# Kernel tuning notes

Measured on AMD Instinct MI355X. Metric: run time of the kernel, lower is better.

## Reference

```python
import jax, jax.numpy as jnp
import numpy as np

B, S, D, H, R = 4, 1024, 1024, 16, 4
HD = D // H
EPS = 1e-5


def layer_norm(x, g, b):
    mu = jnp.mean(x, axis=-1, keepdims=True)
    var = jnp.mean(jnp.square(x - mu), axis=-1, keepdims=True)
    return (x - mu) * jax.lax.rsqrt(var + EPS) * g + b


def setup_inputs() -> dict:
    key = jax.random.key(0)
    ks = jax.random.split(key, 12)
    sd = 1.0 / np.sqrt(D)
    sf = 1.0 / np.sqrt(R * D)
    inp = {
        "x": jax.random.normal(ks[0], (B, S, D), jnp.float32),
        "ln1_g": jnp.ones((D,), jnp.float32),
        "ln1_b": jnp.zeros((D,), jnp.float32),
        "wq": jax.random.uniform(ks[1], (D, D), jnp.float32, -sd, sd),
        "bq": jnp.zeros((D,), jnp.float32),
        "wk": jax.random.uniform(ks[2], (D, D), jnp.float32, -sd, sd),
        "bk": jnp.zeros((D,), jnp.float32),
        "wv": jax.random.uniform(ks[3], (D, D), jnp.float32, -sd, sd),
        "bv": jnp.zeros((D,), jnp.float32),
        "wo": jax.random.uniform(ks[4], (D, D), jnp.float32, -sd, sd),
        "bo": jnp.zeros((D,), jnp.float32),
        "ln2_g": jnp.ones((D,), jnp.float32),
        "ln2_b": jnp.zeros((D,), jnp.float32),
        "w1": jax.random.uniform(ks[5], (D, R * D), jnp.float32, -sd, sd),
        "b1": jnp.zeros((R * D,), jnp.float32),
        "w2": jax.random.uniform(ks[6], (R * D, D), jnp.float32, -sf, sf),
        "b2": jnp.zeros((D,), jnp.float32),
    }
    return inp


def reference(x, ln1_g, ln1_b, wq, bq, wk, bk, wv, bv, wo, bo,
              ln2_g, ln2_b, w1, b1, w2, b2):
    # Pre-LN MHA. Per-head Q/K/V linears concatenated == one batched projection
    # reshaped into heads, so we batch all heads in single GEMMs.
    h = layer_norm(x, ln1_g, ln1_b)
    q = (h @ wq + bq).reshape(B, S, H, HD)
    k = (h @ wk + bk).reshape(B, S, H, HD)
    v = (h @ wv + bv).reshape(B, S, H, HD)
    scores = jnp.einsum("bqhd,bkhd->bhqk", q, k) / np.sqrt(HD)
    attn = jax.nn.softmax(scores, axis=-1)
    ctx = jnp.einsum("bhqk,bkhd->bqhd", attn, v).reshape(B, S, D)
    x = x + ctx @ wo + bo
    # Pre-LN MLP with exact (erf) GELU, matching torch nn.GELU default.
    h2 = layer_norm(x, ln2_g, ln2_b)
    mlp = jax.nn.gelu(h2 @ w1 + b1, approximate=False) @ w2 + b2
    return x + mlp
```

## Files before the change

### kernel.cpp

```cpp
#include <hip/hip_runtime.h>

typedef unsigned short u16;
typedef __attribute__((ext_vector_type(8))) __bf16 bf16x8;
typedef __attribute__((ext_vector_type(4))) float floatx4;

#define FLAG_F32OUT  1
#define FLAG_GELU    2
#define FLAG_PARTIAL 4
#define FLAG_PBF16   8

__device__ __forceinline__ u16 f2bf(float f) {
  union { float f; unsigned u; } un;
  un.f = f;
  unsigned u = un.u;
  u += 0x7fffu + ((u >> 16) & 1u);
  return (u16)(u >> 16);
}

__device__ __forceinline__ float bf2f(u16 h) {
  union { unsigned u; float f; } un;
  un.u = ((unsigned)h) << 16;
  return un.f;
}

__device__ __forceinline__ float gelu_f(float x) {
  float t = 1.5957691216f * (x + 0.044715f * x * x * x);
  return x / (1.0f + __expf(-t));
}

__device__ __forceinline__ floatx4 mfma16(bf16x8 a, bf16x8 b, floatx4 c) {
  return __builtin_amdgcn_mfma_f32_16x16x32_bf16(a, b, c, 0, 0, 0);
}

__device__ __forceinline__ void glds16(const void* g, void* l) {
  __builtin_amdgcn_global_load_lds(
      (__attribute__((address_space(1))) unsigned int*)(void*)g,
      (__attribute__((address_space(3))) unsigned int*)l, 16, 0, 0);
}

__global__ __launch_bounds__(256) void prep_all(
    const float* __restrict__ wq, const float* __restrict__ wk,
    const float* __restrict__ wv, const float* __restrict__ wo,
    const float* __restrict__ w1, const float* __restrict__ w2,
    const float* __restrict__ bq, const float* __restrict__ bk,
    const float* __restrict__ bv,
    u16* __restrict__ wqkvt, u16* __restrict__ wot,
    u16* __restrict__ w1t, u16* __restrict__ w2t,
    float* __restrict__ bqkv,
    const float* __restrict__ x, const float* __restrict__ ln1g,
    const float* __restrict__ ln1b, u16* __restrict__ h) {
  int b = blockIdx.x;
  int tx = threadIdx.x, ty = threadIdx.y;
  int tid = ty * 32 + tx;
  if (b >= 12300) {
    int row = b - 12300;
    const float4* xr = (const float4*)(x + (size_t)row * 1024);
    float4 v = xr[tid];
    float s = v.x + v.y + v.z + v.w;
    float s2 = v.x * v.x + v.y * v.y + v.z * v.z + v.w * v.w;
#pragma unroll
    for (int m = 32; m >= 1; m >>= 1) {
      s += __shfl_xor(s, m, 64);
      s2 += __shfl_xor(s2, m, 64);
    }
    __shared__ float red[8];
    int wave = tid >> 6, lane = tid & 63;
    if (lane == 0) { red[wave] = s; red[4 + wave] = s2; }
    __syncthreads();
    s = red[0] + red[1] + red[2] + red[3];
    s2 = red[4] + red[5] + red[6] + red[7];
    float mu = s * (1.0f / 1024.0f);
    float var = s2 * (1.0f / 1024.0f) - mu * mu;
    float inv = rsqrtf(var + 1e-5f);
    float4 gv = ((const float4*)ln1g)[tid];
    float4 bv2 = ((const float4*)ln1b)[tid];
    ushort4 ov;
    ov.x = f2bf((v.x - mu) * inv * gv.x + bv2.x);
    ov.y = f2bf((v.y - mu) * inv * gv.y + bv2.y);
    ov.z = f2bf((v.z - mu) * inv * gv.z + bv2.z);
    ov.w = f2bf((v.w - mu) * inv * gv.w + bv2.w);
    *(ushort4*)(h + (size_t)row * 1024 + tid * 4) = ov;
    return;
  }
  if (b >= 12288) {
    int i = (b - 12288) * 256 + tid;
    float v = (i < 1024) ? bq[i] * 0.125f
                         : (i < 2048 ? bk[i - 1024] : bv[i - 2048]);
    bqkv[i] = v;
    return;
  }
  const float* W;
  u16* Wt;
  int K, N, bx, by;
  float scale = 1.0f;
  if (b < 4096) {
    int w = b >> 10, t = b & 1023;
    bx = t & 31; by = t >> 5; K = 1024; N = 1024;
    if (w == 0)      { W = wq; Wt = wqkvt;                scale = 0.125f; }
    else if (w == 1) { W = wk; Wt = wqkvt + 1024 * 1024; }
    else if (w == 2) { W = wv; Wt = wqkvt + 2 * 1024 * 1024; }
    else             { W = wo; Wt = wot; }
  } else if (b < 8192) {
    int t = b - 4096;
    bx = t & 127; by = t >> 7; K = 1024; N = 4096; W = w1; Wt = w1t;
  } else {
    int t = b - 8192;
    bx = t & 31; by = t >> 5; K = 4096; N = 1024; W = w2; Wt = w2t;
  }
  __shared__ float tile[32][33];
  int n0 = bx * 32, k0 = by * 32;
#pragma unroll
  for (int i = 0; i < 4; ++i)
    tile[ty + i * 8][tx] = W[(size_t)(k0 + ty + i * 8) * N + n0 + tx];
  __syncthreads();
#pragma unroll
  for (int i = 0; i < 4; ++i)
    Wt[(size_t)(n0 + ty + i * 8) * K + k0 + tx] =
        f2bf(tile[tx][ty + i * 8] * scale);
}

__global__ __launch_bounds__(256, 4) void gemm_bt(
    const u16* __restrict__ A, const u16* __restrict__ Bt,
    const float* __restrict__ bias,
    void* __restrict__ outp, void* __restrict__ outp2,
    int M, int N, int K, int Ks, int flags) {
  __shared__ __align__(16) u16 smem[17408];
  u16* As = smem;
  u16* Bs = smem + 8192;
  int tid = threadIdx.x;
  int lane = tid & 63, wave = tid >> 6;
  int lm = lane & 15, quad = lane >> 4;
  int wm = (wave >> 1) * 64, wn = (wave & 1) * 64;
  int bm = blockIdx.x, bn = blockIdx.y;
  int koff = blockIdx.z * Ks;

  const u16* aP = A + (size_t)(bm * 128 + (tid >> 2)) * K + koff + (tid & 3) * 8;
  const u16* bP = Bt + (size_t)(bn * 128 + (tid >> 2)) * K + koff + (tid & 3) * 8;
  u16* asD = As + tid * 8;
  u16* bsD = Bs + tid * 8;
  size_t rstep = (size_t)64 * K;

  floatx4 acc[4][4];
#pragma unroll
  for (int i = 0; i < 4; ++i)
#pragma unroll
    for (int j = 0; j < 4; ++j) acc[i][j] = (floatx4){0.f, 0.f, 0.f, 0.f};

  glds16(aP, asD);
  glds16(aP + rstep, asD + 2048);
  glds16(bP, bsD);
  glds16(bP + rstep, bsD + 2048);
  aP += 32;
  bP += 32;

  int nIter = Ks >> 5;
  for (int it = 0; it < nIter; it += 2) {
    __syncthreads();
    glds16(aP, asD + 4096);
    glds16(aP + rstep, asD + 4096 + 2048);
    glds16(bP, bsD + 4096);
    glds16(bP + rstep, bsD + 4096 + 2048);
    aP += 32;
    bP += 32;
    {
      bf16x8 af[4], bfr[4];
#pragma unroll
      for (int mi = 0; mi < 4; ++mi)
        af[mi] = *(const bf16x8*)&As[(wm + mi * 16 + lm) * 32 + quad * 8];
#pragma unroll
      for (int ni = 0; ni < 4; ++ni)
        bfr[ni] = *(const bf16x8*)&Bs[(wn + ni * 16 + lm) * 32 + quad * 8];
#pragma unroll
      for (int mi = 0; mi < 4; ++mi)
#pragma unroll
        for (int ni = 0; ni < 4; ++ni)
          acc[mi][ni] = mfma16(af[mi], bfr[ni], acc[mi][ni]);
    }
    __syncthreads();
    if (it + 2 < nIter) {
      glds16(aP, asD);
      glds16(aP + rstep, asD + 2048);
      glds16(bP, bsD);
      glds16(bP + rstep, bsD + 2048);
      aP += 32;
      bP += 32;
    }
    {
      bf16x8 af[4], bfr[4];
#pragma unroll
      for (int mi = 0; mi < 4; ++mi)
        af[mi] = *(const bf16x8*)&As[4096 + (wm + mi * 16 + lm) * 32 + quad * 8];
#pragma unroll
      for (int ni = 0; ni < 4; ++ni)
        bfr[ni] = *(const bf16x8*)&Bs[4096 + (wn + ni * 16 + lm) * 32 + quad * 8];
#pragma unroll
      for (int mi = 0; mi < 4; ++mi)
#pragma unroll
        for (int ni = 0; ni < 4; ++ni)
          acc[mi][ni] = mfma16(af[mi], bfr[ni], acc[mi][ni]);
    }
  }

  bool gelu = (flags & FLAG_GELU) != 0;
  bool part = (flags & FLAG_PARTIAL) != 0;
  bool pbf = (flags & FLAG_PBF16) != 0;
  bool f32p = ((flags & FLAG_F32OUT) != 0) ||
              (part && !(pbf && blockIdx.z > 0));
  void* op;
  if (blockIdx.z == 0)
    op = outp;
  else
    op = (char*)outp2 +
         (size_t)(blockIdx.z - 1) * M * N * (pbf ? 2 : 4);

  if (!f32p) {
    u16* Ct = smem;
    __syncthreads();
#pragma unroll
    for (int ni = 0; ni < 4; ++ni) {
      int col = bn * 128 + wn + ni * 16 + lm;
      float bv = part ? 0.0f : bias[col];
#pragma unroll
      for (int mi = 0; mi < 4; ++mi) {
        int lr0 = wm + mi * 16 + quad * 4;
#pragma unroll
        for (int r = 0; r < 4; ++r) {
          float vv = acc[mi][ni][r] + bv;
          if (gelu) vv = gelu_f(vv);
          Ct[(lr0 + r) * 136 + wn + ni * 16 + lm] = f2bf(vv);
        }
      }
    }
    __syncthreads();
#pragma unroll
    for (int p = 0; p < 8; ++p) {
      int unit = p * 256 + tid;
      int row = unit >> 4, ch = unit & 15;
      uint4 v = *(const uint4*)&Ct[row * 136 + ch * 8];
      *(uint4*)&((u16*)op)[(size_t)(bm * 128 + row) * N + bn * 128 + ch * 8] = v;
    }
  } else {
    float* Cf = (float*)smem;
#pragma unroll
    for (int pp = 0; pp < 2; ++pp) {
      __syncthreads();
      if ((wave >> 1) == pp) {
#pragma unroll
        for (int ni = 0; ni < 4; ++ni) {
          int col = bn * 128 + wn + ni * 16 + lm;
          float bv = part ? 0.0f : bias[col];
#pragma unroll
          for (int mi = 0; mi < 4; ++mi) {
            int lr0 = mi * 16 + quad * 4;
#pragma unroll
            for (int r = 0; r < 4; ++r) {
              float vv = acc[mi][ni][r] + bv;
              if (gelu) vv = gelu_f(vv);
              Cf[(lr0 + r) * 132 + wn + ni * 16 + lm] = vv;
            }
          }
        }
      }
      __syncthreads();
#pragma unroll
      for (int p = 0; p < 8; ++p) {
        int unit = p * 256 + tid;
        int row = unit >> 5, ch = unit & 31;
        float4 v = *(const float4*)&Cf[row * 132 + ch * 4];
        size_t gi = (size_t)(bm * 128 + pp * 64 + row) * N + bn * 128 + ch * 4;
        *(float4*)&((float*)op)[gi] = v;
      }
    }
  }
}

__global__ __launch_bounds__(512) void flash_attn(
    const u16* __restrict__ qkv, u16* __restrict__ ctx) {
  __shared__ __align__(16) u16 Qs[128 * 72];
  __shared__ __align__(16) u16 Ks[64 * 72];
  __shared__ __align__(16) u16 Vt[64 * 64];

  int tid = threadIdx.x;
  int lane = tid & 63, wave = tid >> 6;
  int lm = lane & 15, quad = lane >> 4;
  int qt = blockIdx.x & 7;
  int hh = (blockIdx.x >> 3) & 15;
  int b = blockIdx.x >> 7;

  int krow = tid >> 3;
  int col8 = (tid & 7) * 8;
  int cb = col8 >> 3;

  size_t base_q = ((size_t)(b * 1024 + qt * 128)) * 3072 + hh * 64;
#pragma unroll
  for (int r = 0; r < 2; ++r) {
    int idx = r * 512 + tid;
    int row = idx >> 3;
    int c8 = (idx & 7) * 8;
    *(uint4*)&Qs[row * 72 + c8] =
        *(const uint4*)&qkv[base_q + (size_t)row * 3072 + c8];
  }
  __syncthreads();
  bf16x8 a0 = *(const bf16x8*)&Qs[(wave * 16 + lm) * 72 + quad * 8];
  bf16x8 a1 = *(const bf16x8*)&Qs[(wave * 16 + lm) * 72 + 32 + quad * 8];
  u16* Ps = &Qs[wave * 16 * 72];

  float l_r[4];
  floatx4 acc[4];
#pragma unroll
  for (int r = 0; r < 4; ++r) l_r[r] = 0.0f;
#pragma unroll
  for (int d = 0; d < 4; ++d) acc[d] = (floatx4){0.f, 0.f, 0.f, 0.f};

  size_t kv0 = ((size_t)(b * 1024 + krow)) * 3072 + 1024 + hh * 64 + col8;
  const size_t kv_step = (size_t)64 * 3072;

  uint4 kreg = *(const uint4*)&qkv[kv0];
  uint4 vreg = *(const uint4*)&qkv[kv0 + 1024];

  int rw = krow >> 3;
  int rl = krow & 7;

  for (int j = 0; j < 16; ++j) {
    __syncthreads();
    *(uint4*)&Ks[krow * 72 + col8] = kreg;
    {
      u16* ve = (u16*)&vreg;
#pragma unroll
      for (int e = 0; e < 8; ++e) {
        int d = col8 + e;
        int chunk = (rw ^ cb ^ e) & 7;
        Vt[d * 64 + chunk * 8 + rl] = ve[e];
      }
    }
    __syncthreads();

    if (j < 15) {
      size_t kvn = kv0 + (size_t)(j + 1) * kv_step;
      kreg = *(const uint4*)&qkv[kvn];
      vreg = *(const uint4*)&qkv[kvn + 1024];
    }

    floatx4 sacc[4];
#pragma unroll
    for (int ni = 0; ni < 4; ++ni) {
      bf16x8 b0 = *(const bf16x8*)&Ks[(ni * 16 + lm) * 72 + quad * 8];
      bf16x8 b1 = *(const bf16x8*)&Ks[(ni * 16 + lm) * 72 + 32 + quad * 8];
      floatx4 z = (floatx4){0.f, 0.f, 0.f, 0.f};
      z = mfma16(a0, b0, z);
      z = mfma16(a1, b1, z);
      sacc[ni] = z;
    }

#pragma unroll
    for (int r = 0; r < 4; ++r) {
      float p0 = __expf(sacc[0][r]);
      float p1 = __expf(sacc[1][r]);
      float p2 = __expf(sacc[2][r]);
      float p3 = __expf(sacc[3][r]);
      l_r[r] += (p0 + p1) + (p2 + p3);
      Ps[(quad * 4 + r) * 72 + 0 * 16 + lm] = f2bf(p0);
      Ps[(quad * 4 + r) * 72 + 1 * 16 + lm] = f2bf(p1);
      Ps[(quad * 4 + r) * 72 + 2 * 16 + lm] = f2bf(p2);
      Ps[(quad * 4 + r) * 72 + 3 * 16 + lm] = f2bf(p3);
    }

    bf16x8 pa0 = *(const bf16x8*)&Ps[lm * 72 + quad * 8];
    bf16x8 pa1 = *(const bf16x8*)&Ps[lm * 72 + 32 + quad * 8];
#pragma unroll
    for (int dd = 0; dd < 4; ++dd) {
      int d = dd * 16 + lm;
      int dx = ((d >> 3) ^ d) & 7;
      bf16x8 vb0 = *(const bf16x8*)&Vt[d * 64 + ((quad ^ dx) & 7) * 8];
      bf16x8 vb1 = *(const bf16x8*)&Vt[d * 64 + (((4 + quad) ^ dx) & 7) * 8];
      acc[dd] = mfma16(pa0, vb0, acc[dd]);
      acc[dd] = mfma16(pa1, vb1, acc[dd]);
    }
  }

  float rl4[4];
#pragma unroll
  for (int r = 0; r < 4; ++r) {
    float sm = l_r[r];
#pragma unroll
    for (int mm = 1; mm < 16; mm <<= 1) sm += __shfl_xor(sm, mm, 64);
    rl4[r] = 1.0f / sm;
  }
#pragma unroll
  for (int dd = 0; dd < 4; ++dd)
#pragma unroll
    for (int r = 0; r < 4; ++r)
      Ps[(quad * 4 + r) * 72 + dd * 16 + lm] = f2bf(acc[dd][r] * rl4[r]);
  size_t obase = (size_t)(b * 1024 + qt * 128 + wave * 16);
#pragma unroll
  for (int p = 0; p < 2; ++p) {
    int unit = p * 64 + lane;
    int row = unit >> 3, ch = unit & 7;
    uint4 v = *(const uint4*)&Ps[row * 72 + ch * 8];
    *(uint4*)&ctx[(obase + row) * 1024 + hh * 64 + ch * 8] = v;
  }
}

__global__ __launch_bounds__(256) void reduce_ln(
    float* __restrict__ x2, const float* __restrict__ p1,
    const float* __restrict__ x, const float* __restrict__ bo,
    const float* __restrict__ g, const float* __restrict__ bb,
    u16* __restrict__ h2) {
  int row = blockIdx.x, tid = threadIdx.x;
  size_t base = (size_t)row * 256;
  float4 a = ((const float4*)x2)[base + tid];
  float4 p = ((const float4*)p1)[base + tid];
  float4 c = ((const float4*)x)[base + tid];
  float4 d = ((const float4*)bo)[tid];
  float4 o;
  o.x = a.x + p.x + c.x + d.x;
  o.y = a.y + p.y + c.y + d.y;
  o.z = a.z + p.z + c.z + d.z;
  o.w = a.w + p.w + c.w + d.w;
  ((float4*)x2)[base + tid] = o;

  float s = o.x + o.y + o.z + o.w;
  float s2 = o.x * o.x + o.y * o.y + o.z * o.z + o.w * o.w;
#pragma unroll
  for (int m = 32; m >= 1; m >>= 1) {
    s += __shfl_xor(s, m, 64);
    s2 += __shfl_xor(s2, m, 64);
  }
  __shared__ float red[8];
  int wave = tid >> 6, lane = tid & 63;
  if (lane == 0) { red[wave] = s; red[4 + wave] = s2; }
  __syncthreads();
  s = red[0] + red[1] + red[2] + red[3];
  s2 = red[4] + red[5] + red[6] + red[7];
  float mu = s * (1.0f / 1024.0f);
  float var = s2 * (1.0f / 1024.0f) - mu * mu;
  float inv = rsqrtf(var + 1e-5f);
  float4 gv = ((const float4*)g)[tid];
  float4 bv = ((const float4*)bb)[tid];
  ushort4 ov;
  ov.x = f2bf((o.x - mu) * inv * gv.x + bv.x);
  ov.y = f2bf((o.y - mu) * inv * gv.y + bv.y);
  ov.z = f2bf((o.z - mu) * inv * gv.z + bv.z);
  ov.w = f2bf((o.w - mu) * inv * gv.w + bv.w);
  *(ushort4*)(h2 + (size_t)row * 1024 + tid * 4) = ov;
}

__global__ __launch_bounds__(256) void reduce4b(
    float* __restrict__ out, const u16* __restrict__ pb,
    const float* __restrict__ resid, const float* __restrict__ bias) {
  int i = blockIdx.x * 256 + threadIdx.x;
  float4 a = ((const float4*)out)[i];
  ushort4 q0 = ((const ushort4*)pb)[i];
  ushort4 q1 = ((const ushort4*)(pb + 4194304))[i];
  ushort4 q2 = ((const ushort4*)(pb + 8388608))[i];
  float4 c = ((const float4*)resid)[i];
  float4 d = ((const float4*)bias)[i & 255];
  float4 o;
  o.x = a.x + bf2f(q0.x) + bf2f(q1.x) + bf2f(q2.x) + c.x + d.x;
  o.y = a.y + bf2f(q0.y) + bf2f(q1.y) + bf2f(q2.y) + c.y + d.y;
  o.z = a.z + bf2f(q0.z) + bf2f(q1.z) + bf2f(q2.z) + c.z + d.z;
  o.w = a.w + bf2f(q0.w) + bf2f(q1.w) + bf2f(q2.w) + c.w + d.w;
  ((float4*)out)[i] = o;
}

extern "C" void kernel_launch(void* const* d_in, const int* in_sizes, int n_in,
                              void* d_out, int out_size, void* d_ws, size_t ws_size,
                              hipStream_t stream) {
  const float* x    = (const float*)d_in[0];
  const float* ln1g = (const float*)d_in[1];
  const float* ln1b = (const float*)d_in[2];
  const float* wq   = (const float*)d_in[3];
  const float* bq   = (const float*)d_in[4];
  const float* wk   = (const float*)d_in[5];
  const float* bk   = (const float*)d_in[6];
  const float* wv   = (const float*)d_in[7];
  const float* bv   = (const float*)d_in[8];
  const float* wo   = (const float*)d_in[9];
  const float* bo   = (const float*)d_in[10];
  const float* ln2g = (const float*)d_in[11];
  const float* ln2b = (const float*)d_in[12];
  const float* w1   = (const float*)d_in[13];
  const float* b1   = (const float*)d_in[14];
  const float* w2   = (const float*)d_in[15];
  const float* b2   = (const float*)d_in[16];

  char* ws = (char*)d_ws;
  const size_t MB = 1024ull * 1024ull;
  u16*   h     = (u16*)(ws + 0 * MB);
  u16*   h2    = (u16*)(ws + 0 * MB);
  u16*   qkv   = (u16*)(ws + 8 * MB);
  float* pwo   = (float*)(ws + 8 * MB);
  u16*   act   = (u16*)(ws + 8 * MB);
  u16*   ctxb  = (u16*)(ws + 32 * MB);
  float* bqkv  = (float*)(ws + 32 * MB);
  float* x2    = (float*)(ws + 40 * MB);
  u16*   pw2   = (u16*)(ws + 56 * MB);
  u16*   wqkvt = (u16*)(ws + 64 * MB);
  u16*   wot   = (u16*)(ws + 70 * MB);
  u16*   w1t   = (u16*)(ws + 72 * MB);
  u16*   w2t   = (u16*)(ws + 80 * MB);

  prep_all<<<16396, dim3(32, 8), 0, stream>>>(
      wq, wk, wv, wo, w1, w2, bq, bk, bv, wqkvt, wot, w1t, w2t, bqkv,
      x, ln1g, ln1b, h);

  gemm_bt<<<dim3(32, 24, 1), 256, 0, stream>>>(
      h, wqkvt, bqkv, (void*)qkv, nullptr, 4096, 3072, 1024, 1024, 0);

  flash_attn<<<512, 512, 0, stream>>>(qkv, ctxb);

  gemm_bt<<<dim3(32, 8, 2), 256, 0, stream>>>(
      ctxb, wot, nullptr, (void*)x2, (void*)pwo, 4096, 1024, 1024, 512,
      FLAG_PARTIAL);
  reduce_ln<<<4096, 256, 0, stream>>>(x2, pwo, x, bo, ln2g, ln2b, h2);

  gemm_bt<<<dim3(32, 32, 1), 256, 0, stream>>>(
      h2, w1t, b1, (void*)act, nullptr, 4096, 4096, 1024, 1024, FLAG_GELU);

  gemm_bt<<<dim3(32, 8, 4), 256, 0, stream>>>(
      act, w2t, nullptr, d_out, (void*)pw2, 4096, 1024, 4096, 1024,
      FLAG_PARTIAL | FLAG_PBF16);
  reduce4b<<<4096, 256, 0, stream>>>((float*)d_out, pw2, x2, b2);
}
```

Before: 328.3 us.

## Replace direct global-to-LDS loads with register-staged prefetch in GEMM

The GEMM main loop no longer uses global_load_lds double buffering. It now prefetches the next 64-wide K chunk into registers while the current chunk is computed, writes those registers to LDS at the start of each iteration, and runs two MFMA sub-steps per barrier pair. This hides global latency behind compute through register staging and halves the number of barrier pairs per K. In exchange it adds VGPR pressure and extra LDS store instructions, and the LDS write now sits between the barriers instead of overlapping with the MFMAs.

```diff
diff --git a/kernel.cpp b/kernel.cpp
--- a/kernel.cpp
+++ b/kernel.cpp
@@ -30,12 +30,6 @@
 
 __device__ __forceinline__ floatx4 mfma16(bf16x8 a, bf16x8 b, floatx4 c) {
   return __builtin_amdgcn_mfma_f32_16x16x32_bf16(a, b, c, 0, 0, 0);
-}
-
-__device__ __forceinline__ void glds16(const void* g, void* l) {
-  __builtin_amdgcn_global_load_lds(
-      (__attribute__((address_space(1))) unsigned int*)(void*)g,
-      (__attribute__((address_space(3))) unsigned int*)l, 16, 0, 0);
 }
 
 __global__ __launch_bounds__(256) void prep_all(
@@ -146,53 +140,50 @@
 #pragma unroll
     for (int j = 0; j < 4; ++j) acc[i][j] = (floatx4){0.f, 0.f, 0.f, 0.f};
 
-  glds16(aP, asD);
-  glds16(aP + rstep, asD + 2048);
-  glds16(bP, bsD);
-  glds16(bP + rstep, bsD + 2048);
-  aP += 32;
-  bP += 32;
-
-  int nIter = Ks >> 5;
-  for (int it = 0; it < nIter; it += 2) {
-    __syncthreads();
-    glds16(aP, asD + 4096);
-    glds16(aP + rstep, asD + 4096 + 2048);
-    glds16(bP, bsD + 4096);
-    glds16(bP + rstep, bsD + 4096 + 2048);
-    aP += 32;
-    bP += 32;
-    {
+  uint4 ra0 = *(const uint4*)aP;
+  uint4 ra1 = *(const uint4*)(aP + rstep);
+  uint4 ra2 = *(const uint4*)(aP + 32);
+  uint4 ra3 = *(const uint4*)(aP + 32 + rstep);
+  uint4 rb0 = *(const uint4*)bP;
+  uint4 rb1 = *(const uint4*)(bP + rstep);
+  uint4 rb2 = *(const uint4*)(bP + 32);
+  uint4 rb3 = *(const uint4*)(bP + 32 + rstep);
+  aP += 64;
+  bP += 64;
+
+  int nIter = Ks >> 6;
+  for (int it = 0; it < nIter; ++it) {
+    __syncthreads();
+    *(uint4*)asD = ra0;
+    *(uint4*)(asD + 2048) = ra1;
+    *(uint4*)(asD + 4096) = ra2;
+    *(uint4*)(asD + 4096 + 2048) = ra3;
+    *(uint4*)bsD = rb0;
+    *(uint4*)(bsD + 2048) = rb1;
+    *(uint4*)(bsD + 4096) = rb2;
+    *(uint4*)(bsD + 4096 + 2048) = rb3;
+    if (it + 1 < nIter) {
+      ra0 = *(const uint4*)aP;
+      ra1 = *(const uint4*)(aP + rstep);
+      ra2 = *(const uint4*)(aP + 32);
+      ra3 = *(const uint4*)(aP + 32 + rstep);
+      rb0 = *(const uint4*)bP;
+      rb1 = *(const uint4*)(bP + rstep);
+      rb2 = *(const uint4*)(bP + 32);
+      rb3 = *(const uint4*)(bP + 32 + rstep);
+      aP += 64;
+      bP += 64;
+    }
+    __syncthreads();
+#pragma unroll
+    for (int p = 0; p < 2; ++p) {
       bf16x8 af[4], bfr[4];
 #pragma unroll
       for (int mi = 0; mi < 4; ++mi)
-        af[mi] = *(const bf16x8*)&As[(wm + mi * 16 + lm) * 32 + quad * 8];
+        af[mi] = *(const bf16x8*)&As[p * 4096 + (wm + mi * 16 + lm) * 32 + quad * 8];
 #pragma unroll
       for (int ni = 0; ni < 4; ++ni)
-        bfr[ni] = *(const bf16x8*)&Bs[(wn + ni * 16 + lm) * 32 + quad * 8];
-#pragma unroll
-      for (int mi = 0; mi < 4; ++mi)
-#pragma unroll
-        for (int ni = 0; ni < 4; ++ni)
-          acc[mi][ni] = mfma16(af[mi], bfr[ni], acc[mi][ni]);
-    }
-    __syncthreads();
-    if (it + 2 < nIter) {
-      glds16(aP, asD);
-      glds16(aP + rstep, asD + 2048);
-      glds16(bP, bsD);
-      glds16(bP + rstep, bsD + 2048);
-      aP += 32;
-      bP += 32;
-    }
-    {
-      bf16x8 af[4], bfr[4];
-#pragma unroll
-      for (int mi = 0; mi < 4; ++mi)
-        af[mi] = *(const bf16x8*)&As[4096 + (wm + mi * 16 + lm) * 32 + quad * 8];
-#pragma unroll
-      for (int ni = 0; ni < 4; ++ni)
-        bfr[ni] = *(const bf16x8*)&Bs[4096 + (wn + ni * 16 + lm) * 32 + quad * 8];
+        bfr[ni] = *(const bf16x8*)&Bs[p * 4096 + (wn + ni * 16 + lm) * 32 + quad * 8];
 #pragma unroll
       for (int mi = 0; mi < 4; ++mi)
 #pragma unroll
```

Result: no change. 326.6 us (-0.5%).
